# Kernel optimization log

Hardware: AMD Instinct MI355X
Metric: run time of the kernel (lower is better)

Reference implementation:

```python
import math
import jax, jax.numpy as jnp
import numpy as np

B, N, D = 32, 1025, 768        # batch, tokens (incl. CLS), backbone channels
C, CD, TD = 64, 128, 256       # num_clusters, cluster_dim, token_dim
REG = 0.1
SINKHORN_ITERS = 5


def setup_inputs() -> dict:
    key = jax.random.key(0)
    ks = jax.random.split(key, 9)
    inv = 1.0 / math.sqrt(D)
    return {
        "x": jax.random.normal(ks[0], (B, N, D), dtype=jnp.float32),
        "Wf": jax.random.normal(ks[1], (D, CD), dtype=jnp.float32) * inv,
        "bf": jnp.zeros((CD,), dtype=jnp.float32),
        "Ws": jax.random.normal(ks[2], (D, C), dtype=jnp.float32) * inv,
        "bs": jnp.zeros((C,), dtype=jnp.float32),
        "Wt": jax.random.normal(ks[3], (D, TD), dtype=jnp.float32) * inv,
        "bt": jnp.zeros((TD,), dtype=jnp.float32),
        "anchors": jax.random.normal(ks[4], (C, CD), dtype=jnp.float32) * 0.1,
        "dust_bin": jnp.array(1.0, dtype=jnp.float32),
        "sharpness": jnp.array(5.0, dtype=jnp.float32),
    }


def _sinkhorn_log(log_a, log_b, M, num_iters, reg):
    # log-domain Sinkhorn: M [B, C+1, Nt], log_a [B, C+1], log_b [B, Nt]
    M = M / reg
    u = jnp.zeros_like(log_a)
    v = jnp.zeros_like(log_b)
    for _ in range(num_iters):
        u = log_a - jax.nn.logsumexp(M + v[:, None, :], axis=2)
        v = log_b - jax.nn.logsumexp(M + u[:, :, None], axis=1)
    return M + u[:, :, None] + v[:, None, :]


def reference(x, Wf, bf, Ws, bs, Wt, bt, anchors, dust_bin, sharpness):
    Bx, Nx, _ = x.shape
    n_tok = Nx - 1
    nC = anchors.shape[0]

    t_global = x[:, 0]            # [B, D]
    fi = x[:, 1:]                 # [B, Nt, D]

    f = fi @ Wf + bf              # [B, Nt, CD]
    s = jnp.einsum('bnd,dc->bcn', fi, Ws) + bs[None, :, None]  # [B, C, Nt]
    s = s * sharpness

    dust = jnp.broadcast_to(dust_bin, (Bx, 1, n_tok))
    s_aug = jnp.concatenate([s, dust], axis=1)  # [B, C+1, Nt]

    log_b = jnp.full((Bx, n_tok), -math.log(n_tok), dtype=x.dtype)
    # n_tok (1024) > nC (64): marginals with dustbin absorbing excess mass
    log_a = jnp.concatenate([
        jnp.full((Bx, nC), -math.log(n_tok), dtype=x.dtype),
        jnp.full((Bx, 1), math.log(n_tok - nC) - math.log(n_tok), dtype=x.dtype),
    ], axis=1)

    log_P = _sinkhorn_log(log_a, log_b, s_aug, SINKHORN_ITERS, REG)
    p = jnp.exp(log_P)[:, :-1, :]  # [B, C, Nt], drop dustbin row

    # sum_n p[b,c,n] * (2*f[b,n,d] - anchors[c,d])  == GEMM + rank-1 correction
    v_agg = 2.0 * jnp.einsum('bcn,bnd->bcd', p, f) \
            - p.sum(axis=2)[:, :, None] * anchors[None]  # [B, C, CD]

    v_local = v_agg.reshape(Bx, -1)   # [B, C*CD]
    v_global = t_global @ Wt + bt     # [B, TD]
    f_out = jnp.concatenate([v_global, v_local], axis=-1)
    norm = jnp.maximum(jnp.linalg.norm(f_out, axis=-1, keepdims=True), 1e-12)
    return f_out / norm
```

## Files before the change

kernel.cpp:

```cpp
#include <hip/hip_runtime.h>

typedef unsigned short u16;
typedef __attribute__((ext_vector_type(8))) short bf16x8;
typedef __attribute__((ext_vector_type(8))) short s16x8;
typedef __attribute__((ext_vector_type(4))) float f32x4;
typedef __attribute__((ext_vector_type(4))) short s16x4;

#define OUTW 8448

static __device__ __forceinline__ float bf2f(u16 u) {
    union { unsigned int i; float f; } x; x.i = ((unsigned int)u) << 16; return x.f;
}
static __device__ __forceinline__ u16 f2bf(float f) {
    union { float f; unsigned int i; } x; x.f = f;
    unsigned int lsb = (x.i >> 16) & 1u;
    return (u16)((x.i + 0x7fffu + lsb) >> 16);
}

__global__ __launch_bounds__(512, 2) void k_gemm1(
    const float* __restrict__ x, const float* __restrict__ Wf, const float* __restrict__ bf_,
    const float* __restrict__ Ws, const float* __restrict__ bs_, const float* __restrict__ sharp,
    u16* __restrict__ fT, float* __restrict__ sM)
{
    __shared__ u16 Asm[128][72];
    __shared__ u16 Bsm[192][72];
    const int tid  = threadIdx.x;
    const int lane = tid & 63;
    const int w    = tid >> 6;
    const int b    = blockIdx.x >> 3;
    const int n0   = (blockIdx.x & 7) << 7;
    const float* Abase = x + ((size_t)b * 1025 + 1 + n0) * 768;

    const int arow = tid >> 2;
    const int ac0  = (tid & 3) << 4;
    int   bkg[3]; const float* bptr[3]; int bstr[3]; int bcol[3];
    #pragma unroll
    for (int s = 0; s < 3; ++s) {
        const int idx = tid + s * 512;
        const int kg  = idx / 192;
        const int col = idx - kg * 192;
        bkg[s] = kg; bcol[s] = col;
        if (col < 128) { bptr[s] = Wf + col; bstr[s] = 128; }
        else           { bptr[s] = Ws + (col - 128); bstr[s] = 64; }
    }

    f32x4 acc[4][3] = {};
    const int wm = w >> 2, wn = w & 3;
    const int wr = wm * 64, wc = wn * 48;

    float4 pa[4];
    float  pb[3][8];

    #pragma unroll
    for (int q = 0; q < 4; ++q)
        pa[q] = *(const float4*)(Abase + (size_t)arow * 768 + ac0 + q * 4);
    #pragma unroll
    for (int s = 0; s < 3; ++s)
        #pragma unroll
        for (int j = 0; j < 8; ++j)
            pb[s][j] = bptr[s][(size_t)(bkg[s] * 8 + j) * bstr[s]];

    for (int ks = 0; ks < 12; ++ks) {
        {
            u16 ta[16];
            #pragma unroll
            for (int q = 0; q < 4; ++q) {
                ta[q*4+0] = f2bf(pa[q].x); ta[q*4+1] = f2bf(pa[q].y);
                ta[q*4+2] = f2bf(pa[q].z); ta[q*4+3] = f2bf(pa[q].w);
            }
            *(s16x8*)&Asm[arow][ac0]     = *(const s16x8*)(ta);
            *(s16x8*)&Asm[arow][ac0 + 8] = *(const s16x8*)(ta + 8);
            #pragma unroll
            for (int s = 0; s < 3; ++s) {
                u16 tb[8];
                #pragma unroll
                for (int j = 0; j < 8; ++j) tb[j] = f2bf(pb[s][j]);
                *(s16x8*)&Bsm[bcol[s]][bkg[s] * 8] = *(const s16x8*)(tb);
            }
        }
        __syncthreads();
        if (ks < 11) {
            const int k0 = (ks + 1) * 64;
            #pragma unroll
            for (int q = 0; q < 4; ++q)
                pa[q] = *(const float4*)(Abase + (size_t)arow * 768 + k0 + ac0 + q * 4);
            #pragma unroll
            for (int s = 0; s < 3; ++s)
                #pragma unroll
                for (int j = 0; j < 8; ++j)
                    pb[s][j] = bptr[s][(size_t)(k0 + bkg[s] * 8 + j) * bstr[s]];
        }
        #pragma unroll
        for (int kk = 0; kk < 2; ++kk) {
            const int kb = kk * 32 + ((lane >> 4) << 3);
            bf16x8 af[4], bfr[3];
            #pragma unroll
            for (int mt = 0; mt < 4; ++mt)
                af[mt] = *(const bf16x8*)&Asm[wr + mt * 16 + (lane & 15)][kb];
            #pragma unroll
            for (int nt = 0; nt < 3; ++nt)
                bfr[nt] = *(const bf16x8*)&Bsm[wc + nt * 16 + (lane & 15)][kb];
            #pragma unroll
            for (int mt = 0; mt < 4; ++mt)
                #pragma unroll
                for (int nt = 0; nt < 3; ++nt)
                    acc[mt][nt] = __builtin_amdgcn_mfma_f32_16x16x32_bf16(af[mt], bfr[nt], acc[mt][nt], 0, 0, 0);
        }
        __syncthreads();
    }
    const int rbase = (lane >> 4) << 2;
    const int cl = lane & 15;
    const float sc = sharp[0] * 10.0f;
    #pragma unroll
    for (int mt = 0; mt < 4; ++mt) {
        const int nbase = n0 + wr + mt * 16 + rbase;
        #pragma unroll
        for (int nt = 0; nt < 3; ++nt) {
            const int col16 = wc + nt * 16;
            const int c = col16 + cl;
            if (col16 < 128) {
                const float bias = bf_[c];
                u16 pk[4];
                #pragma unroll
                for (int r = 0; r < 4; ++r) pk[r] = f2bf(acc[mt][nt][r] + bias);
                *(s16x4*)&fT[((size_t)b * 128 + c) * 1024 + nbase] = *(const s16x4*)pk;
            } else {
                const int cm = c - 128;
                const float bias = bs_[cm];
                float4 v;
                v.x = (acc[mt][nt][0] + bias) * sc;
                v.y = (acc[mt][nt][1] + bias) * sc;
                v.z = (acc[mt][nt][2] + bias) * sc;
                v.w = (acc[mt][nt][3] + bias) * sc;
                *(float4*)&sM[((size_t)b * 64 + cm) * 1024 + nbase] = v;
            }
        }
    }
}

__global__ __launch_bounds__(1024, 1) void k_sinkhorn(
    const float* __restrict__ sM, u16* __restrict__ p_out, float* __restrict__ rs_out)
{
    __shared__ u16   Ksm[64][1024];
    __shared__ float betas[1024];
    __shared__ float alph[68];
    const int b   = blockIdx.x;
    const int tid = threadIdx.x;
    const int l   = tid & 63;
    const int w   = tid >> 6;
    const float* Mb = sM + (size_t)b * 64 * 1024;

    #pragma unroll
    for (int i = 0; i < 4; ++i) {
        const int c = w * 4 + i;
        float v[16];
        #pragma unroll
        for (int q = 0; q < 4; ++q)
            *(float4*)(v + q * 4) = *(const float4*)(Mb + (size_t)c * 1024 + l * 16 + q * 4);
        float mx = v[0];
        #pragma unroll
        for (int j = 1; j < 16; ++j) mx = fmaxf(mx, v[j]);
        #pragma unroll
        for (int off = 32; off > 0; off >>= 1) mx = fmaxf(mx, __shfl_xor(mx, off));
        u16 e[16];
        #pragma unroll
        for (int j = 0; j < 16; ++j) e[j] = f2bf(__expf(v[j] - mx));
        *(s16x8*)&Ksm[c][l * 16]     = *(const s16x8*)(e);
        *(s16x8*)&Ksm[c][l * 16 + 8] = *(const s16x8*)(e + 8);
    }
    betas[tid] = 1.0f;
    __syncthreads();

    const float a_c = 1.0f / 1024.0f, a_dust = 960.0f / 1024.0f, b_n = 1.0f / 1024.0f;
    const int r8 = (l & 7) * 8;
    const int cg = w * 8 + (l >> 3);
    const int bwi = (cg & 63) + ((cg >> 6) << 9);

    for (int it = 0; it < 5; ++it) {
        float bb[16];
        #pragma unroll
        for (int j = 0; j < 2; ++j)
            #pragma unroll
            for (int m = 0; m < 8; ++m)
                bb[j * 8 + m] = betas[l + m * 64 + j * 512];
        float sb = 0.f;
        #pragma unroll
        for (int j = 0; j < 16; ++j) sb += bb[j];
        #pragma unroll
        for (int off = 32; off > 0; off >>= 1) sb += __shfl_xor(sb, off);
        #pragma unroll
        for (int i = 0; i < 4; ++i) {
            const int c = w * 4 + i;
            float s = 0.f;
            #pragma unroll
            for (int j = 0; j < 2; ++j) {
                const bf16x8 kr = *(const bf16x8*)&Ksm[c][8 * l + 512 * j];
                #pragma unroll
                for (int m = 0; m < 8; ++m)
                    s += bf2f((u16)kr[m]) * bb[j * 8 + m];
            }
            #pragma unroll
            for (int off = 32; off > 0; off >>= 1) s += __shfl_xor(s, off);
            if (l == 0) alph[c] = a_c / s;
        }
        if (tid == 0) alph[64] = a_dust / sb;
        __syncthreads();
        f32x4 a0 = *(const f32x4*)&alph[r8];
        f32x4 a1 = *(const f32x4*)&alph[r8 + 4];
        const float ad = alph[64];
        float sc8[8] = {};
        #pragma unroll
        for (int i = 0; i < 8; ++i) {
            const bf16x8 kb = *(const bf16x8*)&Ksm[r8 + i][cg * 8];
            const float av = (i < 4) ? a0[i] : a1[i - 4];
            #pragma unroll
            for (int m = 0; m < 8; ++m)
                sc8[m] += bf2f((u16)kb[m]) * av;
        }
        #pragma unroll
        for (int off = 1; off < 8; off <<= 1)
            #pragma unroll
            for (int m = 0; m < 8; ++m)
                sc8[m] += __shfl_xor(sc8[m], off);
        if ((l & 7) == 0) {
            #pragma unroll
            for (int m = 0; m < 8; ++m)
                betas[bwi + m * 64] = b_n / (sc8[m] + ad);
        }
        __syncthreads();
    }

    float bb[16];
    #pragma unroll
    for (int j = 0; j < 2; ++j)
        #pragma unroll
        for (int m = 0; m < 8; ++m)
            bb[j * 8 + m] = betas[l + m * 64 + j * 512];
    #pragma unroll
    for (int i = 0; i < 4; ++i) {
        const int c = w * 4 + i;
        const float ac = alph[c];
        float pv[16]; float s = 0.f;
        #pragma unroll
        for (int j = 0; j < 2; ++j) {
            const bf16x8 kr = *(const bf16x8*)&Ksm[c][8 * l + 512 * j];
            #pragma unroll
            for (int m = 0; m < 8; ++m) {
                const float t = bf2f((u16)kr[m]) * bb[j * 8 + m];
                pv[j * 8 + m] = t; s += t;
            }
        }
        #pragma unroll
        for (int off = 32; off > 0; off >>= 1) s += __shfl_xor(s, off);
        if (l == 0) rs_out[b * 64 + c] = ac * s;
        u16 pk[16];
        #pragma unroll
        for (int j = 0; j < 16; ++j) pk[j] = f2bf(ac * pv[j]);
        u16* pg = p_out + ((size_t)b * 64 + c) * 1024 + 8 * l;
        *(s16x8*)(pg)       = *(const s16x8*)(pk);
        *(s16x8*)(pg + 512) = *(const s16x8*)(pk + 8);
    }
}

__global__ __launch_bounds__(1024, 1) void k_agg(
    const u16* __restrict__ p, const u16* __restrict__ fT,
    const float* __restrict__ rs, const float* __restrict__ anchors,
    float* __restrict__ out)
{
    const int b = blockIdx.x;
    const int tid = threadIdx.x;
    const int lane = tid & 63;
    const int w = tid >> 6;
    const int mt = w & 3;
    const int ng = w >> 2;
    const u16* arow  = p  + ((size_t)b * 64  + mt * 16 + (lane & 15)) * 1024 + ((lane >> 4) << 3);
    const u16* brow0 = fT + ((size_t)b * 128 + ng * 32 + (lane & 15)) * 1024 + ((lane >> 4) << 3);
    const u16* brow1 = brow0 + 16 * 1024;
    f32x4 acc[2] = {};
    for (int ks = 0; ks < 32; ++ks) {
        const int k0 = ks * 32;
        bf16x8 a  = *(const bf16x8*)(arow  + k0);
        bf16x8 b0 = *(const bf16x8*)(brow0 + k0);
        bf16x8 b1 = *(const bf16x8*)(brow1 + k0);
        acc[0] = __builtin_amdgcn_mfma_f32_16x16x32_bf16(a, b0, acc[0], 0, 0, 0);
        acc[1] = __builtin_amdgcn_mfma_f32_16x16x32_bf16(a, b1, acc[1], 0, 0, 0);
    }
    #pragma unroll
    for (int nt = 0; nt < 2; ++nt) {
        const int d = ng * 32 + nt * 16 + (lane & 15);
        #pragma unroll
        for (int r = 0; r < 4; ++r) {
            const int c = mt * 16 + ((lane >> 4) << 2) + r;
            out[(size_t)b * OUTW + 256 + c * 128 + d] = 2.0f * acc[nt][r] - rs[b * 64 + c] * anchors[c * 128 + d];
        }
    }
}

__global__ void k_vglobal(const float* __restrict__ x, const float* __restrict__ Wt,
                          float* __restrict__ vg)
{
    const int kc = blockIdx.x >> 5;
    const int b  = blockIdx.x & 31;
    const int d  = threadIdx.x;
    const float* xr = x  + (size_t)b * (1025 * 768) + kc * 96;
    const float* wp = Wt + (size_t)kc * 96 * 256 + d;
    float acc = 0.f;
    #pragma unroll 8
    for (int k = 0; k < 96; ++k) acc += xr[k] * wp[(size_t)k * 256];
    vg[(size_t)blockIdx.x * 256 + d] = acc;
}

__global__ __launch_bounds__(256) void k_norm(const float* __restrict__ vg, const float* __restrict__ bt,
                                              float* __restrict__ out)
{
    const int b = blockIdx.x;
    const int t = threadIdx.x;
    float vals[33];
    float ss = 0.f;
    {
        float v = bt[t];
        #pragma unroll
        for (int kc = 0; kc < 8; ++kc) v += vg[(size_t)(kc * 32 + b) * 256 + t];
        vals[0] = v; ss += v * v;
    }
    #pragma unroll
    for (int j = 1; j < 33; ++j) {
        const float v = out[(size_t)b * OUTW + j * 256 + t];
        vals[j] = v; ss += v * v;
    }
    #pragma unroll
    for (int off = 32; off > 0; off >>= 1) ss += __shfl_xor(ss, off);
    __shared__ float part[4];
    if ((t & 63) == 0) part[t >> 6] = ss;
    __syncthreads();
    const float tot = part[0] + part[1] + part[2] + part[3];
    const float inv = 1.0f / fmaxf(sqrtf(tot), 1e-12f);
    #pragma unroll
    for (int j = 0; j < 33; ++j)
        out[(size_t)b * OUTW + j * 256 + t] = vals[j] * inv;
}

extern "C" void kernel_launch(void* const* d_in, const int* in_sizes, int n_in,
                              void* d_out, int out_size, void* d_ws, size_t ws_size,
                              hipStream_t stream)
{
    const float* x      = (const float*)d_in[0];
    const float* Wf     = (const float*)d_in[1];
    const float* bf_    = (const float*)d_in[2];
    const float* Ws     = (const float*)d_in[3];
    const float* bs_    = (const float*)d_in[4];
    const float* Wt     = (const float*)d_in[5];
    const float* bt     = (const float*)d_in[6];
    const float* anchors= (const float*)d_in[7];
    const float* sharp  = (const float*)d_in[9];

    char* ws = (char*)d_ws;
    u16*   fT = (u16*)(ws);
    float* sM = (float*)(ws + 8388608);
    u16*   p  = (u16*)(ws + 16777216);
    float* vg = (float*)(ws + 20971520);
    float* rs = (float*)(ws + 21233664);
    float* out = (float*)d_out;

    k_gemm1   <<<dim3(256), 512,  0, stream>>>(x, Wf, bf_, Ws, bs_, sharp, fT, sM);
    k_vglobal <<<dim3(256), 256,  0, stream>>>(x, Wt, vg);
    k_sinkhorn<<<dim3(32),  1024, 0, stream>>>(sM, p, rs);
    k_agg     <<<dim3(32),  1024, 0, stream>>>(p, fT, rs, anchors, out);
    k_norm    <<<dim3(32),  256,  0, stream>>>(vg, bt, out);
}
```

Before: 275.3 us.

## Prepack weights to bf16, shrink GEMM tiles, fuse sinkhorn+agg+norm into one tail kernel

Adds a pre-pass kernel that converts Wf/Ws to a bf16 packed layout, and runs the global-token projection in the same launch. The main GEMM now loads B fragments directly from global into registers with double-buffered A in LDS, uses 64-row tiles and 512 blocks for better occupancy. Sinkhorn, aggregation and normalization are fused into a single kernel that keeps p in a swizzled LDS buffer, which avoids the global round-trips and extra launches. Risks: the tail kernel runs only 32 blocks, and the extra pre-pass adds a serial step.

After: 256.7 us. 1.07x faster.

```diff
diff --git a/kernel.cpp b/kernel.cpp
--- a/kernel.cpp
+++ b/kernel.cpp
@@ -16,107 +16,135 @@
     unsigned int lsb = (x.i >> 16) & 1u;
     return (u16)((x.i + 0x7fffu + lsb) >> 16);
 }
-
-__global__ __launch_bounds__(512, 2) void k_gemm1(
-    const float* __restrict__ x, const float* __restrict__ Wf, const float* __restrict__ bf_,
-    const float* __restrict__ Ws, const float* __restrict__ bs_, const float* __restrict__ sharp,
+static __device__ __forceinline__ int kswz(int r, int c) {
+    return c ^ (((r ^ (r >> 3)) & 7) << 3);
+}
+
+__global__ __launch_bounds__(256) void k_pre(
+    const float* __restrict__ x, const float* __restrict__ Wf, const float* __restrict__ Ws,
+    const float* __restrict__ Wt, u16* __restrict__ Bp, float* __restrict__ vg)
+{
+    const int bid = blockIdx.x, tid = threadIdx.x;
+    if (bid < 12) {
+        __shared__ float Wl[64][193];
+        const int t = bid;
+        #pragma unroll 4
+        for (int i = 0; i < 32; ++i) {
+            const int idx = i * 256 + tid, r = idx >> 7, c = idx & 127;
+            Wl[r][c] = Wf[(size_t)(t * 64 + r) * 128 + c];
+        }
+        #pragma unroll 4
+        for (int i = 0; i < 16; ++i) {
+            const int idx = i * 256 + tid, r = idx >> 6, c = idx & 63;
+            Wl[r][128 + c] = Ws[(size_t)(t * 64 + r) * 64 + c];
+        }
+        __syncthreads();
+        #pragma unroll
+        for (int i = 0; i < 6; ++i) {
+            const int ch = i * 256 + tid, c = ch >> 3, j0 = (ch & 7) << 3;
+            u16 pk[8];
+            #pragma unroll
+            for (int j = 0; j < 8; ++j) pk[j] = f2bf(Wl[j0 + j][c]);
+            *(s16x8*)&Bp[((size_t)t * 192 + c) * 64 + j0] = *(const s16x8*)pk;
+        }
+    } else {
+        const int blk = bid - 12;
+        const int kc = blk >> 5, b = blk & 31, d = tid;
+        const float* xr = x + (size_t)b * (1025 * 768) + kc * 96;
+        const float* wp = Wt + (size_t)kc * 96 * 256 + d;
+        float acc = 0.f;
+        #pragma unroll 8
+        for (int k = 0; k < 96; ++k) acc += xr[k] * wp[(size_t)k * 256];
+        vg[(size_t)blk * 256 + d] = acc;
+    }
+}
+
+__global__ __launch_bounds__(512, 4) void k_gemm1(
+    const float* __restrict__ x, const u16* __restrict__ Bp,
+    const float* __restrict__ bf_, const float* __restrict__ bs_, const float* __restrict__ sharp,
     u16* __restrict__ fT, float* __restrict__ sM)
 {
-    __shared__ u16 Asm[128][72];
-    __shared__ u16 Bsm[192][72];
+    __shared__ u16 Asm[2][64][72];
     const int tid  = threadIdx.x;
     const int lane = tid & 63;
     const int w    = tid >> 6;
-    const int b    = blockIdx.x >> 3;
-    const int n0   = (blockIdx.x & 7) << 7;
+    const int wm   = w >> 2, wn = w & 3;
+    const int b    = blockIdx.x >> 4;
+    const int n0   = (blockIdx.x & 15) << 6;
     const float* Abase = x + ((size_t)b * 1025 + 1 + n0) * 768;
 
-    const int arow = tid >> 2;
-    const int ac0  = (tid & 3) << 4;
-    int   bkg[3]; const float* bptr[3]; int bstr[3]; int bcol[3];
-    #pragma unroll
-    for (int s = 0; s < 3; ++s) {
-        const int idx = tid + s * 512;
-        const int kg  = idx / 192;
-        const int col = idx - kg * 192;
-        bkg[s] = kg; bcol[s] = col;
-        if (col < 128) { bptr[s] = Wf + col; bstr[s] = 128; }
-        else           { bptr[s] = Ws + (col - 128); bstr[s] = 64; }
-    }
-
-    f32x4 acc[4][3] = {};
-    const int wm = w >> 2, wn = w & 3;
-    const int wr = wm * 64, wc = wn * 48;
-
-    float4 pa[4];
-    float  pb[3][8];
-
-    #pragma unroll
-    for (int q = 0; q < 4; ++q)
-        pa[q] = *(const float4*)(Abase + (size_t)arow * 768 + ac0 + q * 4);
-    #pragma unroll
-    for (int s = 0; s < 3; ++s)
-        #pragma unroll
-        for (int j = 0; j < 8; ++j)
-            pb[s][j] = bptr[s][(size_t)(bkg[s] * 8 + j) * bstr[s]];
-
-    for (int ks = 0; ks < 12; ++ks) {
-        {
-            u16 ta[16];
-            #pragma unroll
-            for (int q = 0; q < 4; ++q) {
-                ta[q*4+0] = f2bf(pa[q].x); ta[q*4+1] = f2bf(pa[q].y);
-                ta[q*4+2] = f2bf(pa[q].z); ta[q*4+3] = f2bf(pa[q].w);
+    const int arow = tid >> 3, ak0 = (tid & 7) << 3;
+    const float* aptr = Abase + (size_t)arow * 768 + ak0;
+    const int fk = (lane >> 4) << 3;
+    const u16* bbase = Bp + (size_t)(wn * 48 + (lane & 15)) * 64 + fk;
+
+    f32x4 acc[2][3] = {};
+    float4 pa[2];
+    bf16x8 bcur[6], bnxt[6];
+
+    pa[0] = *(const float4*)(aptr);
+    pa[1] = *(const float4*)(aptr + 4);
+    #pragma unroll
+    for (int nt = 0; nt < 3; ++nt)
+        #pragma unroll
+        for (int kk = 0; kk < 2; ++kk)
+            bcur[nt * 2 + kk] = *(const bf16x8*)(bbase + nt * 1024 + kk * 32);
+    {
+        u16 t8[8];
+        t8[0] = f2bf(pa[0].x); t8[1] = f2bf(pa[0].y); t8[2] = f2bf(pa[0].z); t8[3] = f2bf(pa[0].w);
+        t8[4] = f2bf(pa[1].x); t8[5] = f2bf(pa[1].y); t8[6] = f2bf(pa[1].z); t8[7] = f2bf(pa[1].w);
+        *(s16x8*)&Asm[0][arow][ak0] = *(const s16x8*)t8;
+    }
+    pa[0] = *(const float4*)(aptr + 64);
+    pa[1] = *(const float4*)(aptr + 68);
+    __syncthreads();
+
+    for (int t = 0; t < 12; ++t) {
+        const int cur = t & 1;
+        if (t < 11) {
+            const u16* bp1 = bbase + (size_t)(t + 1) * 12288;
+            #pragma unroll
+            for (int nt = 0; nt < 3; ++nt)
+                #pragma unroll
+                for (int kk = 0; kk < 2; ++kk)
+                    bnxt[nt * 2 + kk] = *(const bf16x8*)(bp1 + nt * 1024 + kk * 32);
+            u16 t8[8];
+            t8[0] = f2bf(pa[0].x); t8[1] = f2bf(pa[0].y); t8[2] = f2bf(pa[0].z); t8[3] = f2bf(pa[0].w);
+            t8[4] = f2bf(pa[1].x); t8[5] = f2bf(pa[1].y); t8[6] = f2bf(pa[1].z); t8[7] = f2bf(pa[1].w);
+            *(s16x8*)&Asm[cur ^ 1][arow][ak0] = *(const s16x8*)t8;
+        }
+        if (t < 10) {
+            const float* ap = aptr + (size_t)(t + 2) * 64;
+            pa[0] = *(const float4*)(ap);
+            pa[1] = *(const float4*)(ap + 4);
+        }
+        #pragma unroll
+        for (int kk = 0; kk < 2; ++kk) {
+            bf16x8 af[2];
+            af[0] = *(const bf16x8*)&Asm[cur][wm * 32 + (lane & 15)][kk * 32 + fk];
+            af[1] = *(const bf16x8*)&Asm[cur][wm * 32 + 16 + (lane & 15)][kk * 32 + fk];
+            #pragma unroll
+            for (int nt = 0; nt < 3; ++nt) {
+                acc[0][nt] = __builtin_amdgcn_mfma_f32_16x16x32_bf16(af[0], bcur[nt * 2 + kk], acc[0][nt], 0, 0, 0);
+                acc[1][nt] = __builtin_amdgcn_mfma_f32_16x16x32_bf16(af[1], bcur[nt * 2 + kk], acc[1][nt], 0, 0, 0);
             }
-            *(s16x8*)&Asm[arow][ac0]     = *(const s16x8*)(ta);
-            *(s16x8*)&Asm[arow][ac0 + 8] = *(const s16x8*)(ta + 8);
-            #pragma unroll
-            for (int s = 0; s < 3; ++s) {
-                u16 tb[8];
-                #pragma unroll
-                for (int j = 0; j < 8; ++j) tb[j] = f2bf(pb[s][j]);
-                *(s16x8*)&Bsm[bcol[s]][bkg[s] * 8] = *(const s16x8*)(tb);
-            }
+        }
+        if (t < 11) {
+            #pragma unroll
+            for (int i = 0; i < 6; ++i) bcur[i] = bnxt[i];
         }
         __syncthreads();
-        if (ks < 11) {
-            const int k0 = (ks + 1) * 64;
-            #pragma unroll
-            for (int q = 0; q < 4; ++q)
-                pa[q] = *(const float4*)(Abase + (size_t)arow * 768 + k0 + ac0 + q * 4);
-            #pragma unroll
-            for (int s = 0; s < 3; ++s)
-                #pragma unroll
-                for (int j = 0; j < 8; ++j)
-                    pb[s][j] = bptr[s][(size_t)(k0 + bkg[s] * 8 + j) * bstr[s]];
-        }
-        #pragma unroll
-        for (int kk = 0; kk < 2; ++kk) {
-            const int kb = kk * 32 + ((lane >> 4) << 3);
-            bf16x8 af[4], bfr[3];
-            #pragma unroll
-            for (int mt = 0; mt < 4; ++mt)
-                af[mt] = *(const bf16x8*)&Asm[wr + mt * 16 + (lane & 15)][kb];
-            #pragma unroll
-            for (int nt = 0; nt < 3; ++nt)
-                bfr[nt] = *(const bf16x8*)&Bsm[wc + nt * 16 + (lane & 15)][kb];
-            #pragma unroll
-            for (int mt = 0; mt < 4; ++mt)
-                #pragma unroll
-                for (int nt = 0; nt < 3; ++nt)
-                    acc[mt][nt] = __builtin_amdgcn_mfma_f32_16x16x32_bf16(af[mt], bfr[nt], acc[mt][nt], 0, 0, 0);
-        }
-        __syncthreads();
-    }
+    }
+
     const int rbase = (lane >> 4) << 2;
     const int cl = lane & 15;
     const float sc = sharp[0] * 10.0f;
     #pragma unroll
-    for (int mt = 0; mt < 4; ++mt) {
-        const int nbase = n0 + wr + mt * 16 + rbase;
+    for (int mt = 0; mt < 2; ++mt) {
+        const int nbase = n0 + wm * 32 + mt * 16 + rbase;
         #pragma unroll
         for (int nt = 0; nt < 3; ++nt) {
-            const int col16 = wc + nt * 16;
+            const int col16 = wn * 48 + nt * 16;
             const int c = col16 + cl;
             if (col16 < 128) {
                 const float bias = bf_[c];
@@ -138,16 +166,17 @@
     }
 }
 
-__global__ __launch_bounds__(1024, 1) void k_sinkhorn(
-    const float* __restrict__ sM, u16* __restrict__ p_out, float* __restrict__ rs_out)
+__global__ __launch_bounds__(1024, 1) void k_tail(
+    const float* __restrict__ sM, const u16* __restrict__ fT,
+    const float* __restrict__ vg, const float* __restrict__ bt,
+    const float* __restrict__ anchors, float* __restrict__ out)
 {
     __shared__ u16   Ksm[64][1024];
     __shared__ float betas[1024];
     __shared__ float alph[68];
-    const int b   = blockIdx.x;
-    const int tid = threadIdx.x;
-    const int l   = tid & 63;
-    const int w   = tid >> 6;
+    __shared__ float rsL[64];
+    __shared__ float sred[16];
+    const int b = blockIdx.x, tid = threadIdx.x, l = tid & 63, w = tid >> 6;
     const float* Mb = sM + (size_t)b * 64 * 1024;
 
     #pragma unroll
@@ -165,15 +194,15 @@
         u16 e[16];
         #pragma unroll
         for (int j = 0; j < 16; ++j) e[j] = f2bf(__expf(v[j] - mx));
-        *(s16x8*)&Ksm[c][l * 16]     = *(const s16x8*)(e);
-        *(s16x8*)&Ksm[c][l * 16 + 8] = *(const s16x8*)(e + 8);
+        *(s16x8*)&Ksm[c][kswz(c, l * 16)]     = *(const s16x8*)(e);
+        *(s16x8*)&Ksm[c][kswz(c, l * 16 + 8)] = *(const s16x8*)(e + 8);
     }
     betas[tid] = 1.0f;
     __syncthreads();
 
     const float a_c = 1.0f / 1024.0f, a_dust = 960.0f / 1024.0f, b_n = 1.0f / 1024.0f;
-    const int r8 = (l & 7) * 8;
-    const int cg = w * 8 + (l >> 3);
+    const int r8  = (l & 7) * 8;
+    const int cg  = w * 8 + (l >> 3);
     const int bwi = (cg & 63) + ((cg >> 6) << 9);
 
     for (int it = 0; it < 5; ++it) {
@@ -194,10 +223,9 @@
             float s = 0.f;
             #pragma unroll
             for (int j = 0; j < 2; ++j) {
-                const bf16x8 kr = *(const bf16x8*)&Ksm[c][8 * l + 512 * j];
+                const bf16x8 kr = *(const bf16x8*)&Ksm[c][kswz(c, 8 * l + 512 * j)];
                 #pragma unroll
-                for (int m = 0; m < 8; ++m)
-                    s += bf2f((u16)kr[m]) * bb[j * 8 + m];
+                for (int m = 0; m < 8; ++m) s += bf2f((u16)kr[m]) * bb[j * 8 + m];
             }
             #pragma unroll
             for (int off = 32; off > 0; off >>= 1) s += __shfl_xor(s, off);
@@ -211,133 +239,105 @@
         float sc8[8] = {};
         #pragma unroll
         for (int i = 0; i < 8; ++i) {
-            const bf16x8 kb = *(const bf16x8*)&Ksm[r8 + i][cg * 8];
+            const bf16x8 kb = *(const bf16x8*)&Ksm[r8 + i][kswz(r8 + i, cg * 8)];
             const float av = (i < 4) ? a0[i] : a1[i - 4];
             #pragma unroll
+            for (int m = 0; m < 8; ++m) sc8[m] += bf2f((u16)kb[m]) * av;
+        }
+        #pragma unroll
+        for (int off = 1; off < 8; off <<= 1)
+            #pragma unroll
+            for (int m = 0; m < 8; ++m) sc8[m] += __shfl_xor(sc8[m], off);
+        if ((l & 7) == 0) {
+            #pragma unroll
+            for (int m = 0; m < 8; ++m) betas[bwi + m * 64] = b_n / (sc8[m] + ad);
+        }
+        __syncthreads();
+    }
+
+    {
+        float bb[16];
+        #pragma unroll
+        for (int j = 0; j < 2; ++j)
+            #pragma unroll
             for (int m = 0; m < 8; ++m)
-                sc8[m] += bf2f((u16)kb[m]) * av;
-        }
-        #pragma unroll
-        for (int off = 1; off < 8; off <<= 1)
-            #pragma unroll
-            for (int m = 0; m < 8; ++m)
-                sc8[m] += __shfl_xor(sc8[m], off);
-        if ((l & 7) == 0) {
-            #pragma unroll
-            for (int m = 0; m < 8; ++m)
-                betas[bwi + m * 64] = b_n / (sc8[m] + ad);
-        }
-        __syncthreads();
-    }
-
-    float bb[16];
-    #pragma unroll
-    for (int j = 0; j < 2; ++j)
-        #pragma unroll
-        for (int m = 0; m < 8; ++m)
-            bb[j * 8 + m] = betas[l + m * 64 + j * 512];
-    #pragma unroll
-    for (int i = 0; i < 4; ++i) {
-        const int c = w * 4 + i;
-        const float ac = alph[c];
-        float pv[16]; float s = 0.f;
-        #pragma unroll
-        for (int j = 0; j < 2; ++j) {
-            const bf16x8 kr = *(const bf16x8*)&Ksm[c][8 * l + 512 * j];
-            #pragma unroll
-            for (int m = 0; m < 8; ++m) {
-                const float t = bf2f((u16)kr[m]) * bb[j * 8 + m];
-                pv[j * 8 + m] = t; s += t;
+                bb[j * 8 + m] = betas[l + m * 64 + j * 512];
+        #pragma unroll
+        for (int i = 0; i < 4; ++i) {
+            const int c = w * 4 + i;
+            const float ac = alph[c];
+            float s = 0.f;
+            u16 pk[16];
+            #pragma unroll
+            for (int j = 0; j < 2; ++j) {
+                const bf16x8 kr = *(const bf16x8*)&Ksm[c][kswz(c, 8 * l + 512 * j)];
+                #pragma unroll
+                for (int m = 0; m < 8; ++m) {
+                    const float tv = bf2f((u16)kr[m]) * bb[j * 8 + m];
+                    s += tv;
+                    pk[j * 8 + m] = f2bf(ac * tv);
+                }
             }
-        }
-        #pragma unroll
-        for (int off = 32; off > 0; off >>= 1) s += __shfl_xor(s, off);
-        if (l == 0) rs_out[b * 64 + c] = ac * s;
-        u16 pk[16];
-        #pragma unroll
-        for (int j = 0; j < 16; ++j) pk[j] = f2bf(ac * pv[j]);
-        u16* pg = p_out + ((size_t)b * 64 + c) * 1024 + 8 * l;
-        *(s16x8*)(pg)       = *(const s16x8*)(pk);
-        *(s16x8*)(pg + 512) = *(const s16x8*)(pk + 8);
-    }
-}
-
-__global__ __launch_bounds__(1024, 1) void k_agg(
-    const u16* __restrict__ p, const u16* __restrict__ fT,
-    const float* __restrict__ rs, const float* __restrict__ anchors,
-    float* __restrict__ out)
-{
-    const int b = blockIdx.x;
-    const int tid = threadIdx.x;
-    const int lane = tid & 63;
-    const int w = tid >> 6;
-    const int mt = w & 3;
-    const int ng = w >> 2;
-    const u16* arow  = p  + ((size_t)b * 64  + mt * 16 + (lane & 15)) * 1024 + ((lane >> 4) << 3);
-    const u16* brow0 = fT + ((size_t)b * 128 + ng * 32 + (lane & 15)) * 1024 + ((lane >> 4) << 3);
+            #pragma unroll
+            for (int off = 32; off > 0; off >>= 1) s += __shfl_xor(s, off);
+            if (l == 0) rsL[c] = ac * s;
+            *(s16x8*)&Ksm[c][kswz(c, 8 * l)]       = *(const s16x8*)(pk);
+            *(s16x8*)&Ksm[c][kswz(c, 8 * l + 512)] = *(const s16x8*)(pk + 8);
+        }
+    }
+    __syncthreads();
+
+    const int mt = w & 3, ng = w >> 2;
+    const int fk = (l >> 4) << 3;
+    const int arow_ = mt * 16 + (l & 15);
+    const u16* brow0 = fT + ((size_t)b * 128 + ng * 32 + (l & 15)) * 1024 + fk;
     const u16* brow1 = brow0 + 16 * 1024;
-    f32x4 acc[2] = {};
+    f32x4 acc2[2] = {};
+    #pragma unroll 4
     for (int ks = 0; ks < 32; ++ks) {
-        const int k0 = ks * 32;
-        bf16x8 a  = *(const bf16x8*)(arow  + k0);
-        bf16x8 b0 = *(const bf16x8*)(brow0 + k0);
-        bf16x8 b1 = *(const bf16x8*)(brow1 + k0);
-        acc[0] = __builtin_amdgcn_mfma_f32_16x16x32_bf16(a, b0, acc[0], 0, 0, 0);
-        acc[1] = __builtin_amdgcn_mfma_f32_16x16x32_bf16(a, b1, acc[1], 0, 0, 0);
-    }
+        const bf16x8 a  = *(const bf16x8*)&Ksm[arow_][kswz(arow_, ks * 32 + fk)];
+        const bf16x8 b0 = *(const bf16x8*)(brow0 + ks * 32);
+        const bf16x8 b1 = *(const bf16x8*)(brow1 + ks * 32);
+        acc2[0] = __builtin_amdgcn_mfma_f32_16x16x32_bf16(a, b0, acc2[0], 0, 0, 0);
+        acc2[1] = __builtin_amdgcn_mfma_f32_16x16x32_bf16(a, b1, acc2[1], 0, 0, 0);
+    }
+
+    float vgv = 0.f, ss = 0.f;
+    if (tid < 256) {
+        float v = bt[tid];
+        #pragma unroll
+        for (int kc = 0; kc < 8; ++kc) v += vg[(size_t)(kc * 32 + b) * 256 + tid];
+        vgv = v; ss = v * v;
+    }
+    float vloc[2][4];
     #pragma unroll
     for (int nt = 0; nt < 2; ++nt) {
-        const int d = ng * 32 + nt * 16 + (lane & 15);
+        const int d = ng * 32 + nt * 16 + (l & 15);
         #pragma unroll
         for (int r = 0; r < 4; ++r) {
-            const int c = mt * 16 + ((lane >> 4) << 2) + r;
-            out[(size_t)b * OUTW + 256 + c * 128 + d] = 2.0f * acc[nt][r] - rs[b * 64 + c] * anchors[c * 128 + d];
-        }
-    }
-}
-
-__global__ void k_vglobal(const float* __restrict__ x, const float* __restrict__ Wt,
-                          float* __restrict__ vg)
-{
-    const int kc = blockIdx.x >> 5;
-    const int b  = blockIdx.x & 31;
-    const int d  = threadIdx.x;
-    const float* xr = x  + (size_t)b * (1025 * 768) + kc * 96;
-    const float* wp = Wt + (size_t)kc * 96 * 256 + d;
-    float acc = 0.f;
-    #pragma unroll 8
-    for (int k = 0; k < 96; ++k) acc += xr[k] * wp[(size_t)k * 256];
-    vg[(size_t)blockIdx.x * 256 + d] = acc;
-}
-
-__global__ __launch_bounds__(256) void k_norm(const float* __restrict__ vg, const float* __restrict__ bt,
-                                              float* __restrict__ out)
-{
-    const int b = blockIdx.x;
-    const int t = threadIdx.x;
-    float vals[33];
-    float ss = 0.f;
-    {
-        float v = bt[t];
-        #pragma unroll
-        for (int kc = 0; kc < 8; ++kc) v += vg[(size_t)(kc * 32 + b) * 256 + t];
-        vals[0] = v; ss += v * v;
-    }
-    #pragma unroll
-    for (int j = 1; j < 33; ++j) {
-        const float v = out[(size_t)b * OUTW + j * 256 + t];
-        vals[j] = v; ss += v * v;
+            const int c = mt * 16 + ((l >> 4) << 2) + r;
+            const float vv = 2.0f * acc2[nt][r] - rsL[c] * anchors[c * 128 + d];
+            vloc[nt][r] = vv; ss += vv * vv;
+        }
     }
     #pragma unroll
     for (int off = 32; off > 0; off >>= 1) ss += __shfl_xor(ss, off);
-    __shared__ float part[4];
-    if ((t & 63) == 0) part[t >> 6] = ss;
+    if (l == 0) sred[w] = ss;
     __syncthreads();
-    const float tot = part[0] + part[1] + part[2] + part[3];
+    float tot = 0.f;
+    #pragma unroll
+    for (int i = 0; i < 16; ++i) tot += sred[i];
     const float inv = 1.0f / fmaxf(sqrtf(tot), 1e-12f);
-    #pragma unroll
-    for (int j = 0; j < 33; ++j)
-        out[(size_t)b * OUTW + j * 256 + t] = vals[j] * inv;
+    if (tid < 256) out[(size_t)b * OUTW + tid] = vgv * inv;
+    #pragma unroll
+    for (int nt = 0; nt < 2; ++nt) {
+        const int d = ng * 32 + nt * 16 + (l & 15);
+        #pragma unroll
+        for (int r = 0; r < 4; ++r) {
+            const int c = mt * 16 + ((l >> 4) << 2) + r;
+            out[(size_t)b * OUTW + 256 + (size_t)c * 128 + d] = vloc[nt][r] * inv;
+        }
+    }
 }
 
 extern "C" void kernel_launch(void* const* d_in, const int* in_sizes, int n_in,
@@ -357,14 +357,11 @@
     char* ws = (char*)d_ws;
     u16*   fT = (u16*)(ws);
     float* sM = (float*)(ws + 8388608);
-    u16*   p  = (u16*)(ws + 16777216);
-    float* vg = (float*)(ws + 20971520);
-    float* rs = (float*)(ws + 21233664);
+    u16*   Bp = (u16*)(ws + 16777216);
+    float* vg = (float*)(ws + 17072128);
     float* out = (float*)d_out;
 
-    k_gemm1   <<<dim3(256), 512,  0, stream>>>(x, Wf, bf_, Ws, bs_, sharp, fT, sM);
-    k_vglobal <<<dim3(256), 256,  0, stream>>>(x, Wt, vg);
-    k_sinkhorn<<<dim3(32),  1024, 0, stream>>>(sM, p, rs);
-    k_agg     <<<dim3(32),  1024, 0, stream>>>(p, fT, rs, anchors, out);
-    k_norm    <<<dim3(32),  256,  0, stream>>>(vg, bt, out);
-}
+    k_pre  <<<dim3(268), 256,  0, stream>>>(x, Wf, Ws, Wt, Bp, vg);
+    k_gemm1<<<dim3(512), 512,  0, stream>>>(x, Bp, bf_, bs_, sharp, fT, sM);
+    k_tail <<<dim3(32),  1024, 0, stream>>>(sM, fT, vg, bt, anchors, out);
+}
```
